# Performance work log

Measured on AMD Instinct MI355X. Metric: run time of the kernel, lower is better.

The kernel has to match this reference:

```python
import jax, jax.numpy as jnp
import numpy as np

BLOCK = 16
H = 16
KV = 4
HPG = H // KV
DH = 64
SCALE = 1.0 / np.sqrt(DH).astype(np.float32)


def setup_inputs() -> dict:
    key = jax.random.key(0)
    ks = jax.random.split(key, 7)
    B, Ldec, Lenc, D = 2, 8192, 4096, 1024
    s = 1.0 / np.sqrt(D).astype(np.float32)
    return {
        "hidden_states": jax.random.normal(ks[0], (B, Ldec, D), jnp.float32),
        "encoder_hidden_states": jax.random.normal(ks[1], (B, Lenc, D), jnp.float32),
        "attention_mask": jax.random.randint(ks[2], (B, Lenc), 0, 2, jnp.int32),
        "Wq": jax.random.normal(ks[3], (D, H * DH), jnp.float32) * s,
        "Wk": jax.random.normal(ks[4], (D, KV * DH), jnp.float32) * s,
        "Wv": jax.random.normal(ks[5], (D, KV * DH), jnp.float32) * s,
        "Wo": jax.random.normal(ks[6], (H * DH, D), jnp.float32) * s,
    }


def reference(hidden_states, encoder_hidden_states, attention_mask, Wq, Wk, Wv, Wo):
    B, Ldec, D = hidden_states.shape
    Lenc = encoder_hidden_states.shape[1]
    pad = (BLOCK - Ldec % BLOCK) % BLOCK
    x = jnp.pad(hidden_states, ((0, 0), (0, pad), (0, 0))) if pad else hidden_states
    nb = (Ldec + pad) // BLOCK
    # mean-pool decoder tokens into blocks: [B, nb, D]
    pooled = x.reshape(B, nb, BLOCK, D).mean(axis=2)
    # projections; GQA: group q heads by kv head (repeat_interleave order)
    q = (pooled @ Wq).reshape(B, nb, KV, HPG, DH)          # [B, nb, KV, HPG, DH]
    k = (encoder_hidden_states @ Wk).reshape(B, Lenc, KV, DH)
    v = (encoder_hidden_states @ Wv).reshape(B, Lenc, KV, DH)
    scores = jnp.einsum("bngqd,blgd->bgqnl", q, k) * SCALE  # [B, KV, HPG, nb, Lenc]
    mask = (attention_mask == 0)[:, None, None, None, :]
    scores = jnp.where(mask, jnp.float32(-1e9), scores)
    attn = jax.nn.softmax(scores, axis=-1)
    out = jnp.einsum("bgqnl,blgd->bngqd", attn, v)          # [B, nb, KV, HPG, DH]
    out = out.reshape(B, nb, H * DH) @ Wo                   # [B, nb, D]
    # broadcast block output back to token level
    unpooled = jnp.broadcast_to(out[:, :, None, :], (B, nb, BLOCK, D)).reshape(B, nb * BLOCK, D)
    return unpooled[:, :Ldec, :]
```

## Files before the change

### kernel.cpp

```cpp
#include <hip/hip_runtime.h>


typedef unsigned short u16;
typedef __attribute__((ext_vector_type(8))) __bf16 bf16x8;
typedef __attribute__((ext_vector_type(4))) float f32x4;
typedef __attribute__((ext_vector_type(4))) _Float16 f16x4;

static __device__ __forceinline__ u16 f2bf(float f) {
    unsigned int u = __float_as_uint(f);
    u = (u + 0x7fffu + ((u >> 16) & 1u)) >> 16;
    return (u16)u;
}
static __device__ __forceinline__ void gload16(const u16* g, u16* l) {
    __builtin_amdgcn_global_load_lds(
        (const __attribute__((address_space(1))) void*)g,
        (__attribute__((address_space(3))) void*)l, 16, 0, 0);
}

__global__ __launch_bounds__(256) void prep_all(const float* __restrict__ enc,
                                                const float* __restrict__ hid,
                                                const int* __restrict__ mask,
                                                const float* __restrict__ Wq,
                                                const float* __restrict__ Wk,
                                                const float* __restrict__ Wv,
                                                const float* __restrict__ Wo,
                                                u16* __restrict__ encb,
                                                u16* __restrict__ poolb,
                                                u16* __restrict__ mh,
                                                u16* __restrict__ Wq_t,
                                                u16* __restrict__ Wkv_t,
                                                u16* __restrict__ Wo_t) {
    int bid = blockIdx.x;
    if (bid < 1024) {
        const int tid = bid * 256 + threadIdx.x;
        const int c4 = tid & 255;
        const int row = tid >> 8;
        const float4* src = (const float4*)(hid + (size_t)row * 16 * 1024) + c4;
        float4 a = src[0];
#pragma unroll
        for (int t = 1; t < 16; ++t) {
            float4 b = src[(size_t)t * 256];
            a.x += b.x; a.y += b.y; a.z += b.z; a.w += b.w;
        }
        ushort4 o;
        o.x = f2bf(a.x * 0.0625f); o.y = f2bf(a.y * 0.0625f);
        o.z = f2bf(a.z * 0.0625f); o.w = f2bf(a.w * 0.0625f);
        *(ushort4*)(poolb + (size_t)row * 1024 + c4 * 4) = o;
    } else if (bid < 3072) {
        const int base = (bid - 1024) * 1024 + threadIdx.x;
        float4 v[4];
#pragma unroll
        for (int j = 0; j < 4; ++j) v[j] = ((const float4*)enc)[base + j * 256];
#pragma unroll
        for (int j = 0; j < 4; ++j) {
            ushort4 o;
            o.x = f2bf(v[j].x); o.y = f2bf(v[j].y);
            o.z = f2bf(v[j].z); o.w = f2bf(v[j].w);
            ((ushort4*)encb)[base + j * 256] = o;
        }
    } else if (bid < 5632) {
        bid -= 3072;
        const float* in; u16* out; int N, nbx, rowoff;
        if (bid < 1024)      { in = Wq; out = Wq_t;  N = 1024; nbx = 32; rowoff = 0; }
        else if (bid < 2048) { in = Wo; out = Wo_t;  N = 1024; nbx = 32; rowoff = 0; bid -= 1024; }
        else if (bid < 2304) { in = Wk; out = Wkv_t; N = 256;  nbx = 8;  rowoff = 0; bid -= 2048; }
        else                 { in = Wv; out = Wkv_t; N = 256;  nbx = 8;  rowoff = 256; bid -= 2304; }
        const int n0 = (bid % nbx) * 32, k0 = (bid / nbx) * 32;
        __shared__ float t[32][33];
        const int tx = threadIdx.x & 31, ty = threadIdx.x >> 5;
#pragma unroll
        for (int i = 0; i < 4; ++i)
            t[ty + 8 * i][tx] = in[(size_t)(k0 + ty + 8 * i) * N + n0 + tx];
        __syncthreads();
#pragma unroll
        for (int i = 0; i < 4; ++i)
            out[(size_t)(rowoff + n0 + ty + 8 * i) * 1024 + k0 + tx] = f2bf(t[tx][ty + 8 * i]);
    } else {
#pragma unroll
        for (int k = 0; k < 32; ++k) {
            const int i = threadIdx.x + 256 * k;
            mh[i] = mask[i] ? (u16)0x3C00 : (u16)0;
        }
    }
}

template <int MODE>
static __device__ __forceinline__ void gemm_core(const u16* __restrict__ A,
                                                 const u16* __restrict__ Bt,
                                                 u16* __restrict__ outQ,
                                                 float* __restrict__ out_f,
                                                 int m0, int n0, int kt0, int nkt,
                                                 u16* sAB) {
    u16* sA = sAB;
    u16* sB = sAB + 64 * 64;
    const int t = threadIdx.x;
    const int w = t >> 6, lane = t & 63, quad = lane >> 4, r16 = lane & 15;
    const int row8 = lane >> 3, seg = lane & 7;

    f32x4 acc[4];
#pragma unroll
    for (int i = 0; i < 4; ++i) acc[i] = (f32x4){0.f, 0.f, 0.f, 0.f};

    for (int kt = kt0; kt < kt0 + nkt; ++kt) {
        const int k0 = kt * 64;
        __syncthreads();
#pragma unroll
        for (int j = 0; j < 2; ++j) {
            const int ra = w * 16 + j * 8;
            gload16(A + (size_t)(m0 + ra + row8) * 1024 + k0 + seg * 8, sA + ra * 64);
            gload16(Bt + (size_t)(n0 + ra + row8) * 1024 + k0 + seg * 8, sB + ra * 64);
        }
        __syncthreads();
#pragma unroll
        for (int kk = 0; kk < 2; ++kk) {
            const bf16x8 af = *(const bf16x8*)(sA + (16 * w + r16) * 64 + kk * 32 + quad * 8);
#pragma unroll
            for (int nt = 0; nt < 4; ++nt) {
                const bf16x8 bfv = *(const bf16x8*)(sB + (nt * 16 + r16) * 64 + kk * 32 + quad * 8);
                acc[nt] = __builtin_amdgcn_mfma_f32_16x16x32_bf16(af, bfv, acc[nt], 0, 0, 0);
            }
        }
    }

    if (MODE == 0) {
#pragma unroll
        for (int nt = 0; nt < 4; ++nt)
#pragma unroll
            for (int r = 0; r < 4; ++r) {
                const int m = m0 + 16 * w + quad * 4 + r;
                const int c = n0 + nt * 16 + r16;
                const int b = m >> 9, nq = m & 511, g = c >> 8, qh = (c >> 6) & 3, d = c & 63;
                outQ[((((size_t)(b * 4 + g) * 4 + qh) * 512 + nq) << 6) + d] =
                    f2bf(acc[nt][r] * 0.180336880f);
            }
    } else {
#pragma unroll
        for (int nt = 0; nt < 4; ++nt)
#pragma unroll
            for (int r = 0; r < 4; ++r) {
                const int m = m0 + 16 * w + quad * 4 + r;
                const int c = n0 + nt * 16 + r16;
                out_f[(size_t)m * 1024 + c] = acc[nt][r];
            }
    }
}

__global__ __launch_bounds__(256) void gemm_qkv(const u16* __restrict__ poolb,
                                                const u16* __restrict__ encb,
                                                const u16* __restrict__ Wq_t,
                                                const u16* __restrict__ Wkv_t,
                                                const int* __restrict__ maskp,
                                                u16* __restrict__ Qa,
                                                u16* __restrict__ Ka,
                                                u16* __restrict__ Va) {
    __shared__ __align__(16) u16 smem[12288];
    const int bx = blockIdx.x;
    if (bx >= 512) {
        const int b = bx - 512;
        gemm_core<0>(poolb, Wq_t, Qa, nullptr, (b >> 4) * 64, (b & 15) * 64, 0, 16, smem);
        return;
    }
    const int m0 = (bx >> 3) * 128, n0 = (bx & 7) * 64;
    u16* sA = smem;
    u16* sB = smem + 128 * 64;
    const int t = threadIdx.x;
    const int w = t >> 6, lane = t & 63, quad = lane >> 4, r16 = lane & 15;
    const int row8 = lane >> 3, seg = lane & 7;

    f32x4 acc[2][4];
#pragma unroll
    for (int i = 0; i < 2; ++i)
#pragma unroll
        for (int nt = 0; nt < 4; ++nt) acc[i][nt] = (f32x4){0.f, 0.f, 0.f, 0.f};

    for (int kt = 0; kt < 16; ++kt) {
        const int k0 = kt * 64;
        __syncthreads();
#pragma unroll
        for (int p = 0; p < 4; ++p) {
            const int ra = p * 32 + w * 8;
            gload16(encb + (size_t)(m0 + ra + row8) * 1024 + k0 + seg * 8, sA + ra * 64);
        }
#pragma unroll
        for (int p = 0; p < 2; ++p) {
            const int ra = p * 32 + w * 8;
            gload16(Wkv_t + (size_t)(n0 + ra + row8) * 1024 + k0 + seg * 8, sB + ra * 64);
        }
        __syncthreads();
#pragma unroll
        for (int kk = 0; kk < 2; ++kk)
#pragma unroll
            for (int i = 0; i < 2; ++i) {
                const bf16x8 af = *(const bf16x8*)(sA + (w * 32 + i * 16 + r16) * 64 + kk * 32 + quad * 8);
#pragma unroll
                for (int nt = 0; nt < 4; ++nt) {
                    const bf16x8 bfv = *(const bf16x8*)(sB + (nt * 16 + r16) * 64 + kk * 32 + quad * 8);
                    acc[i][nt] = __builtin_amdgcn_mfma_f32_16x16x32_bf16(af, bfv, acc[i][nt], 0, 0, 0);
                }
            }
    }

    const bool isV = (n0 >= 256);
    const int g = (isV ? (n0 - 256) : n0) >> 6;
    const int b = m0 >> 12, l0 = m0 & 4095;
    __syncthreads();
    if (isV) {
        u16* sT = smem;
#pragma unroll
        for (int i = 0; i < 2; ++i) {
            float mfl[4];
#pragma unroll
            for (int r = 0; r < 4; ++r)
                mfl[r] = maskp[b * 4096 + l0 + w * 32 + i * 16 + quad * 4 + r] ? 1.f : 0.f;
#pragma unroll
            for (int nt = 0; nt < 4; ++nt)
#pragma unroll
                for (int r = 0; r < 4; ++r) {
                    const int ml = w * 32 + i * 16 + quad * 4 + r, cl = nt * 16 + r16;
                    union { _Float16 h; u16 u; } cv;
                    cv.h = (_Float16)(acc[i][nt][r] * mfl[r]);
                    sT[cl * 136 + ml] = cv.u;
                }
        }
        __syncthreads();
#pragma unroll
        for (int p = 0; p < 4; ++p) {
            const int idx = t + 256 * p, rr = idx >> 4, ch = idx & 15;
            *(int4*)(Va + ((size_t)(b * 4 + g) * 64 + rr) * 4096 + l0 + ch * 8) =
                *(const int4*)(sT + rr * 136 + ch * 8);
        }
    } else {
        u16* sT = smem;
#pragma unroll
        for (int i = 0; i < 2; ++i)
#pragma unroll
            for (int nt = 0; nt < 4; ++nt)
#pragma unroll
                for (int r = 0; r < 4; ++r) {
                    const int ml = w * 32 + i * 16 + quad * 4 + r, cl = nt * 16 + r16;
                    sT[ml * 72 + cl] = f2bf(acc[i][nt][r]);
                }
        __syncthreads();
#pragma unroll
        for (int p = 0; p < 4; ++p) {
            const int idx = t + 256 * p, rr = idx >> 3, ch = idx & 7;
            *(int4*)(Ka + (((size_t)(b * 4 + g) * 4096 + l0 + rr) << 6) + ch * 8) =
                *(const int4*)(sT + rr * 72 + ch * 8);
        }
    }
}

__global__ __launch_bounds__(256) void gemm_o(const u16* __restrict__ attn,
                                              const u16* __restrict__ Wo_t,
                                              float* __restrict__ blkpart) {
    __shared__ __align__(16) u16 smem[8192];
    const int bx = blockIdx.x;
    const int s = bx >> 8, m0 = ((bx >> 4) & 15) * 64, n0 = (bx & 15) * 64;
    gemm_core<3>(attn, Wo_t, nullptr, blkpart + ((size_t)s << 20), m0, n0, s * 4, 4, smem);
}

__global__ __launch_bounds__(256, 4) void flash_attn(const u16* __restrict__ Qa,
                                                     const u16* __restrict__ Ka,
                                                     const u16* __restrict__ Vt,
                                                     const u16* __restrict__ mh,
                                                     float* __restrict__ Opart,
                                                     float* __restrict__ mlpart) {
    const int bx = blockIdx.x;
    const int s16 = bx & 31, rr = bx >> 5;
    const int split = rr & 3, gb = rr >> 2;
    const int g = gb & 3, b = gb >> 2;
    __shared__ __align__(16) u16 sK[64 * 72];
    __shared__ __align__(16) u16 sV[64 * 68];
    const int t = threadIdx.x;
    const int qh = t >> 6, lane = t & 63, quad = lane >> 4, r16 = lane & 15;

    bf16x8 aq[2];
    {
        const size_t qbase = ((((size_t)(b * 4 + g) * 4 + qh) * 512) + s16 * 16 + r16) * 64;
#pragma unroll
        for (int kk = 0; kk < 2; ++kk)
            aq[kk] = *(const bf16x8*)(Qa + qbase + kk * 32 + quad * 8);
    }
    const u16* Kg = Ka + (size_t)(b * 4 + g) * 4096 * 64 + (size_t)split * 1024 * 64;
    const u16* Vg = Vt + (size_t)(b * 4 + g) * 64 * 4096 + split * 1024;
    const u16* mb = mh + b * 4096 + split * 1024 + quad * 4;

    f32x4 o[4], lacc;
#pragma unroll
    for (int i = 0; i < 4; ++i) o[i] = (f32x4){0.f, 0.f, 0.f, 0.f};
    lacc = (f32x4){0.f, 0.f, 0.f, 0.f};

    for (int tile = 0; tile < 16; ++tile) {
        const int l0 = tile * 64;
        __syncthreads();
#pragma unroll
        for (int p = 0; p < 2; ++p) {
            const int idx = t + 256 * p, row = idx >> 3, seg = idx & 7;
            *(int4*)(sK + row * 72 + seg * 8) =
                *(const int4*)(Kg + (size_t)(l0 + row) * 64 + seg * 8);
            *(int4*)(sV + row * 68 + seg * 8) =
                *(const int4*)(Vg + (size_t)row * 4096 + l0 + seg * 8);
        }
        __syncthreads();

        f32x4 st[4];
#pragma unroll
        for (int nt = 0; nt < 4; ++nt) st[nt] = (f32x4){0.f, 0.f, 0.f, 0.f};
#pragma unroll
        for (int kk = 0; kk < 2; ++kk)
#pragma unroll
            for (int nt = 0; nt < 4; ++nt) {
                const bf16x8 ka = *(const bf16x8*)(sK + (nt * 16 + r16) * 72 + kk * 32 + quad * 8);
                st[nt] = __builtin_amdgcn_mfma_f32_16x16x32_bf16(ka, aq[kk], st[nt], 0, 0, 0);
            }

#pragma unroll
        for (int nt = 0; nt < 4; ++nt) {
            f16x4 pa;
#pragma unroll
            for (int j = 0; j < 4; ++j)
                pa[j] = (_Float16)__builtin_amdgcn_exp2f(st[nt][j]);
            const f16x4 bvm = *(const f16x4*)(mb + l0 + nt * 16);
            lacc = __builtin_amdgcn_mfma_f32_16x16x16f16(pa, bvm, lacc, 0, 0, 0);
#pragma unroll
            for (int dt = 0; dt < 4; ++dt) {
                const f16x4 bv = *(const f16x4*)(sV + (dt * 16 + r16) * 68 + nt * 16 + quad * 4);
                o[dt] = __builtin_amdgcn_mfma_f32_16x16x16f16(pa, bv, o[dt], 0, 0, 0);
            }
        }
    }

    const size_t pbase = ((size_t)bx * 4 + qh) * 1024;
#pragma unroll
    for (int dt = 0; dt < 4; ++dt)
#pragma unroll
        for (int r = 0; r < 4; ++r)
            Opart[pbase + (size_t)(quad * 4 + r) * 64 + dt * 16 + r16] = o[dt][r];
    if (r16 == 0) {
#pragma unroll
        for (int r = 0; r < 4; ++r)
            mlpart[((size_t)bx * 4 + qh) * 16 + quad * 4 + r] = lacc[r];
    }
}

__global__ __launch_bounds__(256) void flash_combine(const float* __restrict__ Opart,
                                                     const float* __restrict__ mlpart,
                                                     u16* __restrict__ attnout) {
    const int bx = blockIdx.x;
    const int s16 = bx & 31, h = bx >> 5;
    const int qh = h & 3, g = (h >> 2) & 3, b = h >> 4;
    const int t = threadIdx.x;
    const int q = t >> 4, dg = t & 15;
    float4 a = make_float4(0.f, 0.f, 0.f, 0.f);
    float L = 0.f;
#pragma unroll
    for (int s = 0; s < 4; ++s) {
        const size_t part = (((size_t)((b * 4 + g) * 4 + s) * 32 + s16) * 4 + qh);
        const float4 v = *(const float4*)(Opart + part * 1024 + q * 64 + dg * 4);
        a.x += v.x; a.y += v.y; a.z += v.z; a.w += v.w;
        L += mlpart[part * 16 + q];
    }
    const float invL = 1.f / L;
    ushort4 ov;
    ov.x = f2bf(a.x * invL); ov.y = f2bf(a.y * invL);
    ov.z = f2bf(a.z * invL); ov.w = f2bf(a.w * invL);
    *(ushort4*)(attnout + ((size_t)b * 512 + s16 * 16 + q) * 1024 +
                (g * 4 + qh) * 64 + dg * 4) = ov;
}

__global__ __launch_bounds__(256) void bcast_out(const float* __restrict__ blkpart,
                                                 float* __restrict__ out) {
    const int tid = blockIdx.x * 256 + threadIdx.x;
    const int c4 = tid & 255;
    const int row = tid >> 8;
    float4 a = make_float4(0.f, 0.f, 0.f, 0.f);
#pragma unroll
    for (int s = 0; s < 4; ++s) {
        const float4 v = ((const float4*)blkpart)[(s << 18) + (row << 8) + c4];
        a.x += v.x; a.y += v.y; a.z += v.z; a.w += v.w;
    }
    const int b = row >> 9, n = row & 511;
    float4* dst = (float4*)out + (((size_t)b * 8192 + n * 16) << 8) + c4;
#pragma unroll
    for (int rep = 0; rep < 16; ++rep)
        dst[(size_t)rep << 8] = a;
}

extern "C" void kernel_launch(void* const* d_in, const int* in_sizes, int n_in,
                              void* d_out, int out_size, void* d_ws, size_t ws_size,
                              hipStream_t stream) {
    const float* hid  = (const float*)d_in[0];
    const float* enc  = (const float*)d_in[1];
    const int*   mask = (const int*)d_in[2];
    const float* Wq   = (const float*)d_in[3];
    const float* Wk   = (const float*)d_in[4];
    const float* Wv   = (const float*)d_in[5];
    const float* Wo   = (const float*)d_in[6];
    float* out = (float*)d_out;

    char* ws = (char*)d_ws;
    size_t off = 0;
    auto alloc = [&](size_t bytes) -> char* {
        char* p = ws + off;
        off += (bytes + 255) & ~(size_t)255;
        return p;
    };
    u16* Wq_t  = (u16*)alloc((size_t)1024 * 1024 * 2);
    u16* Wkv_t = (u16*)alloc((size_t)512 * 1024 * 2);
    u16* Wo_t  = (u16*)alloc((size_t)1024 * 1024 * 2);
    u16* encb  = (u16*)alloc((size_t)8192 * 1024 * 2);
    u16* poolb = (u16*)alloc((size_t)1024 * 1024 * 2);
    u16* Qa    = (u16*)alloc((size_t)1024 * 1024 * 2);
    u16* Ka    = (u16*)alloc((size_t)8 * 4096 * 64 * 2);
    u16* Va    = (u16*)alloc((size_t)8 * 4096 * 64 * 2);
    u16* attn  = (u16*)alloc((size_t)1024 * 1024 * 2);
    u16* mh    = (u16*)alloc((size_t)8192 * 2);
    float* Opart   = (float*)encb;
    float* blkpart = (float*)encb;
    float* mlpart  = (float*)poolb;

    prep_all<<<5633, 256, 0, stream>>>(enc, hid, mask, Wq, Wk, Wv, Wo,
                                       encb, poolb, mh, Wq_t, Wkv_t, Wo_t);
    gemm_qkv<<<768, 256, 0, stream>>>(poolb, encb, Wq_t, Wkv_t, mask, Qa, Ka, Va);
    flash_attn<<<1024, 256, 0, stream>>>(Qa, Ka, Va, mh, Opart, mlpart);
    flash_combine<<<1024, 256, 0, stream>>>(Opart, mlpart, attn);
    gemm_o<<<1024, 256, 0, stream>>>(attn, Wo_t, blkpart);
    bcast_out<<<1024, 256, 0, stream>>>(blkpart, out);
}
```

Measured before the change: 243.6 us.

## Fuse split-K reductions into producer kernels via last-block atomic counters

Removes the separate flash_combine and bcast_out launches. The last block to finish for each tile, detected with an atomic counter plus thread fences, now does the split reduction, the normalization and the broadcast write inside flash_attn and gemm_o. The counters are zeroed in prep_all. Block-index mappings in gemm_qkv and flash_attn are also permuted, likely to improve cache locality. This cuts two kernel launches and their inter-kernel gaps, but the reduction work is concentrated in a quarter of the blocks, which causes tail imbalance.

```diff
diff --git a/kernel.cpp b/kernel.cpp
--- a/kernel.cpp
+++ b/kernel.cpp
@@ -2,6 +2,7 @@
 
 
 typedef unsigned short u16;
+typedef unsigned int u32;
 typedef __attribute__((ext_vector_type(8))) __bf16 bf16x8;
 typedef __attribute__((ext_vector_type(4))) float f32x4;
 typedef __attribute__((ext_vector_type(4))) _Float16 f16x4;
@@ -29,7 +30,9 @@
                                                 u16* __restrict__ mh,
                                                 u16* __restrict__ Wq_t,
                                                 u16* __restrict__ Wkv_t,
-                                                u16* __restrict__ Wo_t) {
+                                                u16* __restrict__ Wo_t,
+                                                u32* __restrict__ cntF,
+                                                u32* __restrict__ cntO) {
     int bid = blockIdx.x;
     if (bid < 1024) {
         const int tid = bid * 256 + threadIdx.x;
@@ -81,6 +84,8 @@
             const int i = threadIdx.x + 256 * k;
             mh[i] = mask[i] ? (u16)0x3C00 : (u16)0;
         }
+        cntF[threadIdx.x] = 0;
+        cntO[threadIdx.x] = 0;
     }
 }
 
@@ -160,7 +165,8 @@
         gemm_core<0>(poolb, Wq_t, Qa, nullptr, (b >> 4) * 64, (b & 15) * 64, 0, 16, smem);
         return;
     }
-    const int m0 = (bx >> 3) * 128, n0 = (bx & 7) * 64;
+    const int mt = (bx & 7) + 8 * ((bx >> 3) & 7);
+    const int m0 = mt * 128, n0 = (bx >> 6) * 64;
     u16* sA = smem;
     u16* sB = smem + 128 * 64;
     const int t = threadIdx.x;
@@ -250,27 +256,21 @@
     }
 }
 
-__global__ __launch_bounds__(256) void gemm_o(const u16* __restrict__ attn,
-                                              const u16* __restrict__ Wo_t,
-                                              float* __restrict__ blkpart) {
-    __shared__ __align__(16) u16 smem[8192];
-    const int bx = blockIdx.x;
-    const int s = bx >> 8, m0 = ((bx >> 4) & 15) * 64, n0 = (bx & 15) * 64;
-    gemm_core<3>(attn, Wo_t, nullptr, blkpart + ((size_t)s << 20), m0, n0, s * 4, 4, smem);
-}
-
 __global__ __launch_bounds__(256, 4) void flash_attn(const u16* __restrict__ Qa,
                                                      const u16* __restrict__ Ka,
                                                      const u16* __restrict__ Vt,
                                                      const u16* __restrict__ mh,
                                                      float* __restrict__ Opart,
-                                                     float* __restrict__ mlpart) {
+                                                     float* __restrict__ mlpart,
+                                                     u16* __restrict__ attnout,
+                                                     u32* __restrict__ cntF) {
     const int bx = blockIdx.x;
-    const int s16 = bx & 31, rr = bx >> 5;
+    const int s16 = bx >> 5, rr = bx & 31;
     const int split = rr & 3, gb = rr >> 2;
     const int g = gb & 3, b = gb >> 2;
     __shared__ __align__(16) u16 sK[64 * 72];
     __shared__ __align__(16) u16 sV[64 * 68];
+    __shared__ int sLast;
     const int t = threadIdx.x;
     const int qh = t >> 6, lane = t & 63, quad = lane >> 4, r16 = lane & 15;
 
@@ -341,49 +341,70 @@
         for (int r = 0; r < 4; ++r)
             mlpart[((size_t)bx * 4 + qh) * 16 + quad * 4 + r] = lacc[r];
     }
-}
-
-__global__ __launch_bounds__(256) void flash_combine(const float* __restrict__ Opart,
-                                                     const float* __restrict__ mlpart,
-                                                     u16* __restrict__ attnout) {
+
+    __threadfence();
+    __syncthreads();
+    if (t == 0) sLast = (atomicAdd(&cntF[gb * 32 + s16], 1) == 3);
+    __syncthreads();
+    if (!sLast) return;
+    __threadfence();
+
+    const int q = t >> 4, dg = t & 15;
+#pragma unroll
+    for (int qqh = 0; qqh < 4; ++qqh) {
+        float4 a = make_float4(0.f, 0.f, 0.f, 0.f);
+        float L = 0.f;
+#pragma unroll
+        for (int s = 0; s < 4; ++s) {
+            const size_t part = ((size_t)((gb * 4 + s) + 32 * s16) * 4 + qqh);
+            const float4 v = *(const float4*)(Opart + part * 1024 + q * 64 + dg * 4);
+            a.x += v.x; a.y += v.y; a.z += v.z; a.w += v.w;
+            L += mlpart[part * 16 + q];
+        }
+        const float invL = 1.f / L;
+        ushort4 ov;
+        ov.x = f2bf(a.x * invL); ov.y = f2bf(a.y * invL);
+        ov.z = f2bf(a.z * invL); ov.w = f2bf(a.w * invL);
+        *(ushort4*)(attnout + ((size_t)b * 512 + s16 * 16 + q) * 1024 +
+                    (g * 4 + qqh) * 64 + dg * 4) = ov;
+    }
+}
+
+__global__ __launch_bounds__(256) void gemm_o(const u16* __restrict__ attn,
+                                              const u16* __restrict__ Wo_t,
+                                              float* __restrict__ blkpart,
+                                              float* __restrict__ out,
+                                              u32* __restrict__ cntO) {
+    __shared__ __align__(16) u16 smem[8192];
+    __shared__ int sLast;
     const int bx = blockIdx.x;
-    const int s16 = bx & 31, h = bx >> 5;
-    const int qh = h & 3, g = (h >> 2) & 3, b = h >> 4;
+    const int s = bx >> 8, mn = bx & 255;
+    const int m0 = ((bx >> 4) & 15) * 64, n0 = (bx & 15) * 64;
+    gemm_core<3>(attn, Wo_t, nullptr, blkpart + ((size_t)s << 20), m0, n0, s * 4, 4, smem);
+
     const int t = threadIdx.x;
-    const int q = t >> 4, dg = t & 15;
-    float4 a = make_float4(0.f, 0.f, 0.f, 0.f);
-    float L = 0.f;
-#pragma unroll
-    for (int s = 0; s < 4; ++s) {
-        const size_t part = (((size_t)((b * 4 + g) * 4 + s) * 32 + s16) * 4 + qh);
-        const float4 v = *(const float4*)(Opart + part * 1024 + q * 64 + dg * 4);
-        a.x += v.x; a.y += v.y; a.z += v.z; a.w += v.w;
-        L += mlpart[part * 16 + q];
-    }
-    const float invL = 1.f / L;
-    ushort4 ov;
-    ov.x = f2bf(a.x * invL); ov.y = f2bf(a.y * invL);
-    ov.z = f2bf(a.z * invL); ov.w = f2bf(a.w * invL);
-    *(ushort4*)(attnout + ((size_t)b * 512 + s16 * 16 + q) * 1024 +
-                (g * 4 + qh) * 64 + dg * 4) = ov;
-}
-
-__global__ __launch_bounds__(256) void bcast_out(const float* __restrict__ blkpart,
-                                                 float* __restrict__ out) {
-    const int tid = blockIdx.x * 256 + threadIdx.x;
-    const int c4 = tid & 255;
-    const int row = tid >> 8;
-    float4 a = make_float4(0.f, 0.f, 0.f, 0.f);
-#pragma unroll
-    for (int s = 0; s < 4; ++s) {
-        const float4 v = ((const float4*)blkpart)[(s << 18) + (row << 8) + c4];
-        a.x += v.x; a.y += v.y; a.z += v.z; a.w += v.w;
-    }
-    const int b = row >> 9, n = row & 511;
-    float4* dst = (float4*)out + (((size_t)b * 8192 + n * 16) << 8) + c4;
-#pragma unroll
-    for (int rep = 0; rep < 16; ++rep)
-        dst[(size_t)rep << 8] = a;
+    __threadfence();
+    __syncthreads();
+    if (t == 0) sLast = (atomicAdd(&cntO[mn], 1) == 3);
+    __syncthreads();
+    if (!sLast) return;
+    __threadfence();
+
+#pragma unroll
+    for (int j = 0; j < 4; ++j) {
+        const int idx = t + 256 * j, rowl = idx >> 4, c4l = idx & 15;
+        float4 a = make_float4(0.f, 0.f, 0.f, 0.f);
+#pragma unroll
+        for (int ss = 0; ss < 4; ++ss) {
+            const float4 v = ((const float4*)blkpart)[(ss << 18) + ((m0 + rowl) << 8) + (n0 >> 2) + c4l];
+            a.x += v.x; a.y += v.y; a.z += v.z; a.w += v.w;
+        }
+        const int m = m0 + rowl, b = m >> 9, n = m & 511;
+        float4* dst = (float4*)out + (((size_t)b * 8192 + n * 16) << 8) + (n0 >> 2) + c4l;
+#pragma unroll
+        for (int rep = 0; rep < 16; ++rep)
+            dst[(size_t)rep << 8] = a;
+    }
 }
 
 extern "C" void kernel_launch(void* const* d_in, const int* in_sizes, int n_in,
@@ -415,15 +436,15 @@
     u16* Va    = (u16*)alloc((size_t)8 * 4096 * 64 * 2);
     u16* attn  = (u16*)alloc((size_t)1024 * 1024 * 2);
     u16* mh    = (u16*)alloc((size_t)8192 * 2);
+    u32* cntF  = (u32*)alloc(256 * 4);
+    u32* cntO  = (u32*)alloc(256 * 4);
     float* Opart   = (float*)encb;
     float* blkpart = (float*)encb;
     float* mlpart  = (float*)poolb;
 
     prep_all<<<5633, 256, 0, stream>>>(enc, hid, mask, Wq, Wk, Wv, Wo,
-                                       encb, poolb, mh, Wq_t, Wkv_t, Wo_t);
+                                       encb, poolb, mh, Wq_t, Wkv_t, Wo_t, cntF, cntO);
     gemm_qkv<<<768, 256, 0, stream>>>(poolb, encb, Wq_t, Wkv_t, mask, Qa, Ka, Va);
-    flash_attn<<<1024, 256, 0, stream>>>(Qa, Ka, Va, mh, Opart, mlpart);
-    flash_combine<<<1024, 256, 0, stream>>>(Opart, mlpart, attn);
-    gemm_o<<<1024, 256, 0, stream>>>(attn, Wo_t, blkpart);
-    bcast_out<<<1024, 256, 0, stream>>>(blkpart, out);
-}
+    flash_attn<<<1024, 256, 0, stream>>>(Qa, Ka, Va, mh, Opart, mlpart, attn, cntF);
+    gemm_o<<<1024, 256, 0, stream>>>(attn, Wo_t, blkpart, out, cntO);
+}
```

Result: slower. 616.5 us (+153.0%).
